# Performance work log

Measured on AMD Instinct MI355X. Metric: run time of the kernel, lower is better.

## Reference

```python
import jax, jax.numpy as jnp
import numpy as np

C = 256      # channel_num
K = 9        # key_num
B, H, W = 8, 64, 64


def setup_inputs() -> dict:
    key = jax.random.key(0)
    ks = jax.random.split(key, 12)
    s = 1.0 / np.sqrt(C)
    return {
        "query_layer": jax.random.normal(ks[0], (B, C, H, W), jnp.float32),
        "key_layer": jax.random.normal(ks[1], (B, C, H, W), jnp.float32),
        "gumbel_noise": jax.random.gumbel(ks[2], (B, K, H, W), jnp.float32),
        "w_refer": jax.random.normal(ks[3], (C, C), jnp.float32) * s,
        "b_refer": jax.random.normal(ks[4], (C,), jnp.float32) * 0.01,
        "w_attn": jax.random.normal(ks[5], (K, C), jnp.float32) * s,
        "b_attn": jax.random.normal(ks[6], (K,), jnp.float32) * 0.01,
        "w_mask": jax.random.normal(ks[7], (K, C), jnp.float32) * s,
        "b_mask": jax.random.normal(ks[8], (K,), jnp.float32) * 0.01,
        "w_off": jax.random.normal(ks[9], (2 * K, C), jnp.float32) * 0.02,
        "b_off": jax.random.normal(ks[10], (2 * K,), jnp.float32) * 0.01,
        "temp": 1,
    }


def _conv1x1(w, b, x):
    # w: (O,C), x: (B,C,H,W) -> (B,O,H,W)
    return jnp.einsum('oc,bchw->bohw', w, x) + b[None, :, None, None]


def _sample_one(img, py, px):
    # img: (C,H,W); py,px: (K,H,W) absolute sampling coords (bilinear, zero pad)
    h, w = img.shape[1], img.shape[2]
    y0 = jnp.floor(py)
    x0 = jnp.floor(px)
    wy = py - y0          # weight toward y0+1
    wx = px - x0

    def gather(yi, xi):
        valid = (yi >= 0) & (yi < h) & (xi >= 0) & (xi < w)
        yc = jnp.clip(yi, 0, h - 1).astype(jnp.int32)
        xc = jnp.clip(xi, 0, w - 1).astype(jnp.int32)
        return img[:, yc, xc] * valid[None].astype(img.dtype)  # (C,K,H,W)

    out = (gather(y0, x0) * ((1 - wy) * (1 - wx))[None]
           + gather(y0, x0 + 1) * ((1 - wy) * wx)[None]
           + gather(y0 + 1, x0) * (wy * (1 - wx))[None]
           + gather(y0 + 1, x0 + 1) * (wy * wx)[None])
    return out  # (C,K,H,W)


def reference(query_layer, key_layer, gumbel_noise, w_refer, b_refer,
              w_attn, b_attn, w_mask, b_mask, w_off, b_off, temp):
    key_feature = _conv1x1(w_refer, b_refer, key_layer)          # (B,C,H,W)
    attn_weights = _conv1x1(w_attn, b_attn, query_layer)         # (B,K,H,W)
    soft_mask = _conv1x1(w_mask, b_mask, query_layer)            # (B,K,H,W)
    # gumbel_softmax(hard=False) over key dim
    hard_mask = jax.nn.softmax((soft_mask + gumbel_noise) / temp, axis=1)
    offset = _conv1x1(w_off, b_off, query_layer)                 # (B,2K,H,W)

    # faithful to offset[:, i:i+2]: overlapping (dy,dx) slices
    dy = offset[:, 0:K]        # (B,K,H,W)
    dx = offset[:, 1:K + 1]    # (B,K,H,W)
    ys = jnp.arange(H, dtype=offset.dtype)[None, None, :, None]
    xs = jnp.arange(W, dtype=offset.dtype)[None, None, None, :]
    py = ys + dy
    px = xs + dx

    sampled = jax.vmap(_sample_one)(key_feature, py, px)         # (B,C,K,H,W)

    aw = jax.nn.softmax(attn_weights * hard_mask, axis=1)        # (B,K,H,W)
    out = jnp.einsum('bkhw,bckhw->bchw', aw, sampled)            # (B,C,H,W)
    return out
```

## Files before the change

### kernel.cpp

```cpp
#include <hip/hip_runtime.h>

typedef unsigned short u16;
typedef __attribute__((ext_vector_type(8))) short bf16x8;
typedef __attribute__((ext_vector_type(4))) float f32x4;

__device__ __forceinline__ u16 f2bf(float f) {
    unsigned u = __float_as_uint(f);
    unsigned r = (u + 0x7fffu + ((u >> 16) & 1u)) >> 16;
    return (u16)r;
}
__device__ __forceinline__ float bf2f(u16 h) {
    union { unsigned u; float f; } x; x.u = ((unsigned)h) << 16; return x.f;
}

#define NB 8
#define NC 256
#define NK 9
#define NH 64
#define NW 64
#define NP 4096
#define BAND 320
#define SB_STRIDE 328

__global__ __launch_bounds__(256) void kf_gemm(const float* __restrict__ key,
                                               const float* __restrict__ w_refer,
                                               const float* __restrict__ b_refer,
                                               u16* __restrict__ kf16)
{
    const int bid = blockIdx.x;
    const int b   = bid & 7;
    const int p0  = (bid >> 3) << 6;
    const int lane = threadIdx.x & 63, wid = threadIdx.x >> 6;
    const int fr = lane & 15, kq = (lane >> 4) << 3;
    const int co0w = wid << 6;

    f32x4 acc[4][4];
    #pragma unroll
    for (int i = 0; i < 4; ++i)
        #pragma unroll
        for (int j = 0; j < 4; ++j) acc[i][j] = (f32x4){0.f, 0.f, 0.f, 0.f};

    const float* kb = &key[(size_t)b * NC * NP + p0];

    for (int ks = 0; ks < 8; ++ks) {
        const int k0 = (ks << 5) + kq;
        bf16x8 af[4], bfv[4];
        #pragma unroll
        for (int mi = 0; mi < 4; ++mi) {
            const float* src = &w_refer[(size_t)(co0w + (mi << 4) + fr) * NC + k0];
            float4 v0 = *(const float4*)src;
            float4 v1 = *(const float4*)(src + 4);
            bf16x8 a;
            a[0] = (short)f2bf(v0.x); a[1] = (short)f2bf(v0.y);
            a[2] = (short)f2bf(v0.z); a[3] = (short)f2bf(v0.w);
            a[4] = (short)f2bf(v1.x); a[5] = (short)f2bf(v1.y);
            a[6] = (short)f2bf(v1.z); a[7] = (short)f2bf(v1.w);
            af[mi] = a;
        }
        #pragma unroll
        for (int ni = 0; ni < 4; ++ni) {
            const float* src = &kb[(size_t)k0 * NP + (ni << 4) + fr];
            bf16x8 bv;
            #pragma unroll
            for (int j = 0; j < 8; ++j) bv[j] = (short)f2bf(src[(size_t)j * NP]);
            bfv[ni] = bv;
        }
        #pragma unroll
        for (int mi = 0; mi < 4; ++mi)
            #pragma unroll
            for (int ni = 0; ni < 4; ++ni)
                acc[mi][ni] = __builtin_amdgcn_mfma_f32_16x16x32_bf16(af[mi], bfv[ni], acc[mi][ni], 0, 0, 0);
    }

    const int col = lane & 15, rbase = (lane >> 4) << 2;
    #pragma unroll
    for (int mi = 0; mi < 4; ++mi) {
        #pragma unroll
        for (int rr = 0; rr < 4; ++rr) {
            int co = co0w + (mi << 4) + rbase + rr;
            float bias = b_refer[co];
            u16* dst = &kf16[((size_t)b * NC + co) * NP + p0 + col];
            #pragma unroll
            for (int ni = 0; ni < 4; ++ni)
                dst[ni << 4] = f2bf(acc[mi][ni][rr] + bias);
        }
    }
}

__global__ __launch_bounds__(256) void head_meta(const float* __restrict__ query,
                                                 const float* __restrict__ gumbel,
                                                 const float* __restrict__ w_attn, const float* __restrict__ b_attn,
                                                 const float* __restrict__ w_mask, const float* __restrict__ b_mask,
                                                 const float* __restrict__ w_off,  const float* __restrict__ b_off,
                                                 const int* __restrict__ temp_p,
                                                 float4* __restrict__ wgt, uint2* __restrict__ offs)
{
    __shared__ u16 A[48][264];
    __shared__ float hdT[128][41];
    const int pt = blockIdx.x;
    const int b  = pt & 7;
    const int p0 = (pt >> 3) << 7;
    const int t = threadIdx.x;
    const int lane = t & 63, wn = t >> 6;
    const int fr = lane & 15, kq = (lane >> 4) << 3;

    for (int i = t; i < 1152; i += 256) {
        int o = i >> 5, c = (i & 31) << 3;
        const float* src = (o < 9) ? &w_attn[o * NC + c]
                       : (o < 18 ? &w_mask[(o - 9) * NC + c]
                                 : &w_off[(o - 18) * NC + c]);
        float4 v0 = *(const float4*)src;
        float4 v1 = *(const float4*)(src + 4);
        bf16x8 a;
        a[0] = (short)f2bf(v0.x); a[1] = (short)f2bf(v0.y);
        a[2] = (short)f2bf(v0.z); a[3] = (short)f2bf(v0.w);
        a[4] = (short)f2bf(v1.x); a[5] = (short)f2bf(v1.y);
        a[6] = (short)f2bf(v1.z); a[7] = (short)f2bf(v1.w);
        *(bf16x8*)&A[o][c] = a;
    }
    for (int i = t; i < 384; i += 256) {
        bf16x8 z = {0,0,0,0,0,0,0,0};
        *(bf16x8*)&A[36 + (i >> 5)][(i & 31) << 3] = z;
    }
    __syncthreads();

    f32x4 acc[3][2];
    #pragma unroll
    for (int i = 0; i < 3; ++i)
        #pragma unroll
        for (int j = 0; j < 2; ++j) acc[i][j] = (f32x4){0.f, 0.f, 0.f, 0.f};

    for (int ks = 0; ks < 8; ++ks) {
        const int k0 = (ks << 5) + kq;
        bf16x8 af[3], bfv[2];
        #pragma unroll
        for (int mi = 0; mi < 3; ++mi)
            af[mi] = *(const bf16x8*)&A[(mi << 4) + fr][k0];
        #pragma unroll
        for (int ni = 0; ni < 2; ++ni) {
            const float* src = &query[((size_t)b * NC + k0) * NP + p0 + (wn << 5) + (ni << 4) + fr];
            bf16x8 bv;
            #pragma unroll
            for (int j = 0; j < 8; ++j) bv[j] = (short)f2bf(src[(size_t)j * NP]);
            bfv[ni] = bv;
        }
        #pragma unroll
        for (int mi = 0; mi < 3; ++mi)
            #pragma unroll
            for (int ni = 0; ni < 2; ++ni)
                acc[mi][ni] = __builtin_amdgcn_mfma_f32_16x16x32_bf16(af[mi], bfv[ni], acc[mi][ni], 0, 0, 0);
    }
    const int col = lane & 15, rbase = (lane >> 4) << 2;
    #pragma unroll
    for (int mi = 0; mi < 3; ++mi) {
        #pragma unroll
        for (int rr = 0; rr < 4; ++rr) {
            int o = (mi << 4) + rbase + rr;
            if (o < 36) {
                float bias = (o < 9) ? b_attn[o] : (o < 18) ? b_mask[o - 9] : b_off[o - 18];
                #pragma unroll
                for (int ni = 0; ni < 2; ++ni)
                    hdT[(wn << 5) + (ni << 4) + col][o] = acc[mi][ni][rr] + bias;
            }
        }
    }
    __syncthreads();

    if (t < 128) {
        const int pxg = p0 + t;
        const int row = pxg >> 6, xcol = pxg & 63;
        float v[36];
        #pragma unroll
        for (int o = 0; o < 36; ++o) v[o] = hdT[t][o];

        int ti = temp_p[0];
        float tempf = (ti >= 1 && ti < (1 << 23)) ? (float)ti : __int_as_float(ti);
        float am[9], hs[9];
        float mx = -1e30f;
        #pragma unroll
        for (int k = 0; k < 9; ++k) {
            am[k] = v[k];
            float g = gumbel[((size_t)b * NK + k) * NP + pxg];
            hs[k] = (v[9 + k] + g) / tempf;
            mx = fmaxf(mx, hs[k]);
        }
        float ssum = 0.f;
        #pragma unroll
        for (int k = 0; k < 9; ++k) { hs[k] = __expf(hs[k] - mx); ssum += hs[k]; }
        float inv = 1.f / ssum;
        float lg[9]; float mx2 = -1e30f;
        #pragma unroll
        for (int k = 0; k < 9; ++k) { lg[k] = am[k] * (hs[k] * inv); mx2 = fmaxf(mx2, lg[k]); }
        float s2 = 0.f;
        #pragma unroll
        for (int k = 0; k < 9; ++k) { lg[k] = __expf(lg[k] - mx2); s2 += lg[k]; }
        float inv2 = 1.f / s2;
        #pragma unroll
        for (int k = 0; k < 9; ++k) {
            float a = lg[k] * inv2;
            float pyv = (float)row  + v[18 + k];
            float pxv = (float)xcol + v[19 + k];
            float y0f = floorf(pyv), x0f = floorf(pxv);
            float wy = pyv - y0f, wx = pxv - x0f;
            int y0 = (int)y0f, x0 = (int)x0f;
            int y1 = y0 + 1, x1 = x0 + 1;
            float vy0 = (y0 >= 0 && y0 < NH) ? 1.f : 0.f;
            float vy1 = (y1 >= 0 && y1 < NH) ? 1.f : 0.f;
            float vx0 = (x0 >= 0 && x0 < NW) ? 1.f : 0.f;
            float vx1 = (x1 >= 0 && x1 < NW) ? 1.f : 0.f;
            int y0c = min(max(y0, 0), NH - 1), y1c = min(max(y1, 0), NH - 1);
            int x0c = min(max(x0, 0), NW - 1), x1c = min(max(x1, 0), NW - 1);
            unsigned o00 = (unsigned)(y0c * NW + x0c), o01 = (unsigned)(y0c * NW + x1c);
            unsigned o10 = (unsigned)(y1c * NW + x0c), o11 = (unsigned)(y1c * NW + x1c);
            size_t idx = ((size_t)b * NK + k) * NP + pxg;
            wgt[idx]  = make_float4(a * (1.f - wy) * (1.f - wx) * vy0 * vx0,
                                    a * (1.f - wy) * wx * vy0 * vx1,
                                    a * wy * (1.f - wx) * vy1 * vx0,
                                    a * wy * wx * vy1 * vx1);
            offs[idx] = make_uint2(o00 | (o01 << 16), o10 | (o11 << 16));
        }
    }
}

__global__ __launch_bounds__(512, 4) void sample_pass(const u16* __restrict__ kf16,
                                                      const float4* __restrict__ wgt,
                                                      const uint2* __restrict__ offs,
                                                      float* __restrict__ out)
{
    __shared__ float Sf[64][BAND];

    const int bid = blockIdx.x;
    const int b = bid & 7, row = bid >> 3;
    const int t = threadIdx.x;
    const int lane = t & 63, wid = t >> 6;
    const int fr = lane & 15, kq = (lane >> 4) << 3;
    const int c0 = wid << 5;
    const int ylo = min(max(row - 2, 0), NH - 5);
    const int base = ylo << 6;
    const u16* kfb = kf16 + (size_t)b * NC * NP + base;

    bf16x8 apre[4][2];
    #pragma unroll
    for (int s = 0; s < 4; ++s)
        #pragma unroll
        for (int mi = 0; mi < 2; ++mi)
            apre[s][mi] = *(const bf16x8*)&kfb[(size_t)(c0 + (mi << 4) + fr) * NP + (s << 5) + kq];

    const int px = t & 63, kg = t >> 6;
    size_t idx0 = ((size_t)b * NK + kg) * NP + (row << 6) + px;
    float4 wv0 = wgt[idx0];
    uint2  ov0 = offs[idx0];
    float4 wv1 = make_float4(0.f, 0.f, 0.f, 0.f);
    uint2  ov1 = make_uint2(0u, 0u);
    if (kg == 0) {
        size_t idx1 = ((size_t)b * NK + 8) * NP + (row << 6) + px;
        wv1 = wgt[idx1]; ov1 = offs[idx1];
    }

    #pragma unroll
    for (int i = 0; i < 10; ++i)
        ((float4*)Sf)[t + (i << 9)] = (float4){0.f, 0.f, 0.f, 0.f};
    __syncthreads();

    bool esc = false;
    #pragma unroll
    for (int s = 0; s < 2; ++s) {
        if (s == 1 && kg != 0) break;
        float4 wv = s ? wv1 : wv0;
        uint2  ov = s ? ov1 : ov0;
        int   o4[4] = { (int)(ov.x & 0xffffu), (int)(ov.x >> 16),
                        (int)(ov.y & 0xffffu), (int)(ov.y >> 16) };
        float w4[4] = { wv.x, wv.y, wv.z, wv.w };
        #pragma unroll
        for (int c = 0; c < 4; ++c) {
            int u = o4[c] - base;
            if ((unsigned)u < (unsigned)BAND) atomicAdd(&Sf[px][u], w4[c]);
            else esc = true;
        }
    }
    __syncthreads();

    u16* Sb = (u16*)&Sf[0][0];
    bf16x8 pk[5]; int po[5];
    #pragma unroll
    for (int r = 0; r < 5; ++r) {
        int i = t + (r << 9);
        int p = i / 40, j = (i % 40) << 3;
        float4 a = *(const float4*)&Sf[p][j];
        float4 c = *(const float4*)&Sf[p][j + 4];
        bf16x8 q;
        q[0] = (short)f2bf(a.x); q[1] = (short)f2bf(a.y);
        q[2] = (short)f2bf(a.z); q[3] = (short)f2bf(a.w);
        q[4] = (short)f2bf(c.x); q[5] = (short)f2bf(c.y);
        q[6] = (short)f2bf(c.z); q[7] = (short)f2bf(c.w);
        pk[r] = q; po[r] = p * SB_STRIDE + j;
    }
    __syncthreads();
    #pragma unroll
    for (int r = 0; r < 5; ++r)
        *(bf16x8*)&Sb[po[r]] = pk[r];
    __syncthreads();

    f32x4 acc[2][4];
    #pragma unroll
    for (int i = 0; i < 2; ++i)
        #pragma unroll
        for (int j = 0; j < 4; ++j) acc[i][j] = (f32x4){0.f, 0.f, 0.f, 0.f};

    #pragma unroll
    for (int step = 0; step < 10; ++step) {
        bf16x8 a0 = apre[step & 3][0], a1 = apre[step & 3][1];
        if (step + 4 < 10) {
            #pragma unroll
            for (int mi = 0; mi < 2; ++mi)
                apre[step & 3][mi] =
                    *(const bf16x8*)&kfb[(size_t)(c0 + (mi << 4) + fr) * NP + ((step + 4) << 5) + kq];
        }
        bf16x8 bfv[4];
        #pragma unroll
        for (int ni = 0; ni < 4; ++ni)
            bfv[ni] = *(const bf16x8*)&Sb[((ni << 4) + fr) * SB_STRIDE + (step << 5) + kq];
        #pragma unroll
        for (int ni = 0; ni < 4; ++ni) {
            acc[0][ni] = __builtin_amdgcn_mfma_f32_16x16x32_bf16(a0, bfv[ni], acc[0][ni], 0, 0, 0);
            acc[1][ni] = __builtin_amdgcn_mfma_f32_16x16x32_bf16(a1, bfv[ni], acc[1][ni], 0, 0, 0);
        }
    }

    const int col = lane & 15, rbase = (lane >> 4) << 2;
    float* ob = out + (size_t)b * NC * NP + (row << 6);
    #pragma unroll
    for (int mi = 0; mi < 2; ++mi) {
        #pragma unroll
        for (int rr = 0; rr < 4; ++rr) {
            int c = c0 + (mi << 4) + rbase + rr;
            #pragma unroll
            for (int ni = 0; ni < 4; ++ni)
                ob[(size_t)c * NP + (ni << 4) + col] = acc[mi][ni][rr];
        }
    }

    __syncthreads();
    if (esc) {
        for (int s = 0; s < (kg == 0 ? 2 : 1); ++s) {
            int k = s ? 8 : kg;
            size_t idx = ((size_t)b * NK + k) * NP + (row << 6) + px;
            float4 wv = wgt[idx];
            uint2  ov = offs[idx];
            int   o4[4] = { (int)(ov.x & 0xffffu), (int)(ov.x >> 16),
                            (int)(ov.y & 0xffffu), (int)(ov.y >> 16) };
            float w4[4] = { wv.x, wv.y, wv.z, wv.w };
            for (int c = 0; c < 4; ++c) {
                int u = o4[c] - base;
                if ((unsigned)u >= (unsigned)BAND) {
                    for (int cc = 0; cc < NC; ++cc)
                        atomicAdd(&ob[(size_t)cc * NP + px],
                                  w4[c] * bf2f(kf16[((size_t)b * NC + cc) * NP + o4[c]]));
                }
            }
        }
    }
}

extern "C" void kernel_launch(void* const* d_in, const int* in_sizes, int n_in,
                              void* d_out, int out_size, void* d_ws, size_t ws_size,
                              hipStream_t stream)
{
    const float* query   = (const float*)d_in[0];
    const float* key     = (const float*)d_in[1];
    const float* gumbel  = (const float*)d_in[2];
    const float* w_refer = (const float*)d_in[3];
    const float* b_refer = (const float*)d_in[4];
    const float* w_attn  = (const float*)d_in[5];
    const float* b_attn  = (const float*)d_in[6];
    const float* w_mask  = (const float*)d_in[7];
    const float* b_mask  = (const float*)d_in[8];
    const float* w_off   = (const float*)d_in[9];
    const float* b_off   = (const float*)d_in[10];
    const int*   temp    = (const int*)d_in[11];
    float* out = (float*)d_out;

    char* ws = (char*)d_ws;
    u16*    kf16 = (u16*)ws;
    float4* wgt  = (float4*)(ws + (size_t)NB * NP * NC * 2);
    uint2*  offs = (uint2*)((char*)wgt + (size_t)NB * NK * NP * 16);

    kf_gemm<<<512, 256, 0, stream>>>(key, w_refer, b_refer, kf16);
    head_meta<<<256, 256, 0, stream>>>(query, gumbel, w_attn, b_attn, w_mask, b_mask,
                                       w_off, b_off, temp, wgt, offs);
    sample_pass<<<512, 512, 0, stream>>>(kf16, wgt, offs, out);
}
```

Baseline: 67.16 us.

## Fuse GEMM, head and sampling passes into one cooperative kernel with grid sync

Merges the three launches (key-feature GEMM, head/meta computation, banded sampling GEMM) into a single cooperative kernel of 256 blocks by 512 threads. A grid-wide sync presumably separates producing kf16/wgt/offs from consuming them. The key tile is now staged through LDS before bf16 conversion, and each block handles two rows in the sampling phase. This removes launch gaps and inter-kernel drains, but cuts the grid to 256 blocks with large LDS, adds grid-sync cost, and lowers parallelism per phase.

```diff
diff --git a/kernel.cpp b/kernel.cpp
--- a/kernel.cpp
+++ b/kernel.cpp
@@ -1,4 +1,7 @@
 #include <hip/hip_runtime.h>
+#include <hip/hip_cooperative_groups.h>
+
+namespace cg = cooperative_groups;
 
 typedef unsigned short u16;
 typedef __attribute__((ext_vector_type(8))) short bf16x8;
@@ -21,33 +24,106 @@
 #define NP 4096
 #define BAND 320
 #define SB_STRIDE 328
-
-__global__ __launch_bounds__(256) void kf_gemm(const float* __restrict__ key,
-                                               const float* __restrict__ w_refer,
-                                               const float* __restrict__ b_refer,
-                                               u16* __restrict__ kf16)
+#define KF_STR 68
+
+__global__ __launch_bounds__(512, 2) void fused(const float* __restrict__ key,
+                                                const float* __restrict__ query,
+                                                const float* __restrict__ gumbel,
+                                                const float* __restrict__ w_refer,
+                                                const float* __restrict__ b_refer,
+                                                const float* __restrict__ w_attn, const float* __restrict__ b_attn,
+                                                const float* __restrict__ w_mask, const float* __restrict__ b_mask,
+                                                const float* __restrict__ w_off,  const float* __restrict__ b_off,
+                                                const int* __restrict__ temp_p,
+                                                u16* __restrict__ kf16,
+                                                float4* __restrict__ wgt, uint2* __restrict__ offs,
+                                                float* __restrict__ out)
 {
-    const int bid = blockIdx.x;
-    const int b   = bid & 7;
-    const int p0  = (bid >> 3) << 6;
-    const int lane = threadIdx.x & 63, wid = threadIdx.x >> 6;
+    __shared__ __align__(16) char smem[81920];
+    const int bid = blockIdx.x, t = threadIdx.x;
+    const int b = bid & 7, seg = bid >> 3;
+    const int lane = t & 63;
     const int fr = lane & 15, kq = (lane >> 4) << 3;
-    const int co0w = wid << 6;
-
-    f32x4 acc[4][4];
-    #pragma unroll
-    for (int i = 0; i < 4; ++i)
-        #pragma unroll
-        for (int j = 0; j < 4; ++j) acc[i][j] = (f32x4){0.f, 0.f, 0.f, 0.f};
-
-    const float* kb = &key[(size_t)b * NC * NP + p0];
-
-    for (int ks = 0; ks < 8; ++ks) {
-        const int k0 = (ks << 5) + kq;
-        bf16x8 af[4], bfv[4];
-        #pragma unroll
-        for (int mi = 0; mi < 4; ++mi) {
-            const float* src = &w_refer[(size_t)(co0w + (mi << 4) + fr) * NC + k0];
+    const int col = lane & 15, rbase = (lane >> 4) << 2;
+
+    {
+        float* Kf = (float*)smem;
+        const int w = t >> 6;
+        const int co0 = w << 5;
+        #pragma unroll
+        for (int tile = 0; tile < 2; ++tile) {
+            const int p0 = ((seg << 1) + tile) << 6;
+            if (tile) __syncthreads();
+            #pragma unroll
+            for (int i = 0; i < 8; ++i) {
+                int idx = (i << 9) + t;
+                int k = idx >> 4, px4 = (idx & 15) << 2;
+                float4 v = *(const float4*)&key[((size_t)b * NC + k) * NP + p0 + px4];
+                *(float4*)&Kf[k * KF_STR + px4] = v;
+            }
+            __syncthreads();
+
+            f32x4 acc[2][4];
+            #pragma unroll
+            for (int i = 0; i < 2; ++i)
+                #pragma unroll
+                for (int j = 0; j < 4; ++j) acc[i][j] = (f32x4){0.f, 0.f, 0.f, 0.f};
+
+            for (int ks = 0; ks < 8; ++ks) {
+                const int k0 = (ks << 5) + kq;
+                bf16x8 af[2], bfv[4];
+                #pragma unroll
+                for (int mi = 0; mi < 2; ++mi) {
+                    const float* src = &w_refer[(size_t)(co0 + (mi << 4) + fr) * NC + k0];
+                    float4 v0 = *(const float4*)src;
+                    float4 v1 = *(const float4*)(src + 4);
+                    bf16x8 a;
+                    a[0] = (short)f2bf(v0.x); a[1] = (short)f2bf(v0.y);
+                    a[2] = (short)f2bf(v0.z); a[3] = (short)f2bf(v0.w);
+                    a[4] = (short)f2bf(v1.x); a[5] = (short)f2bf(v1.y);
+                    a[6] = (short)f2bf(v1.z); a[7] = (short)f2bf(v1.w);
+                    af[mi] = a;
+                }
+                #pragma unroll
+                for (int ni = 0; ni < 4; ++ni) {
+                    const float* src = &Kf[(size_t)k0 * KF_STR + (ni << 4) + fr];
+                    bf16x8 bv;
+                    #pragma unroll
+                    for (int j = 0; j < 8; ++j) bv[j] = (short)f2bf(src[j * KF_STR]);
+                    bfv[ni] = bv;
+                }
+                #pragma unroll
+                for (int mi = 0; mi < 2; ++mi)
+                    #pragma unroll
+                    for (int ni = 0; ni < 4; ++ni)
+                        acc[mi][ni] = __builtin_amdgcn_mfma_f32_16x16x32_bf16(af[mi], bfv[ni], acc[mi][ni], 0, 0, 0);
+            }
+            #pragma unroll
+            for (int mi = 0; mi < 2; ++mi) {
+                #pragma unroll
+                for (int rr = 0; rr < 4; ++rr) {
+                    int co = co0 + (mi << 4) + rbase + rr;
+                    float bias = b_refer[co];
+                    u16* dst = &kf16[((size_t)b * NC + co) * NP + p0 + col];
+                    #pragma unroll
+                    for (int ni = 0; ni < 4; ++ni)
+                        dst[ni << 4] = f2bf(acc[mi][ni][rr] + bias);
+                }
+            }
+        }
+    }
+    __syncthreads();
+
+    {
+        u16   (*A)[264]  = (u16(*)[264])smem;
+        float (*hdT)[41] = (float(*)[41])(smem + 25344);
+        const int p0h = seg << 7;
+
+        for (int i = t; i < 1152; i += 512) {
+            int o = i >> 5, c = (i & 31) << 3;
+            const float* src = (o < 9) ? &w_attn[o * NC + c]
+                           : (o < 18 ? &w_mask[(o - 9) * NC + c]
+                                     : &w_off[(o - 18) * NC + c]);
             float4 v0 = *(const float4*)src;
             float4 v1 = *(const float4*)(src + 4);
             bf16x8 a;
@@ -55,307 +131,234 @@
             a[2] = (short)f2bf(v0.z); a[3] = (short)f2bf(v0.w);
             a[4] = (short)f2bf(v1.x); a[5] = (short)f2bf(v1.y);
             a[6] = (short)f2bf(v1.z); a[7] = (short)f2bf(v1.w);
-            af[mi] = a;
-        }
-        #pragma unroll
-        for (int ni = 0; ni < 4; ++ni) {
-            const float* src = &kb[(size_t)k0 * NP + (ni << 4) + fr];
-            bf16x8 bv;
-            #pragma unroll
-            for (int j = 0; j < 8; ++j) bv[j] = (short)f2bf(src[(size_t)j * NP]);
-            bfv[ni] = bv;
-        }
-        #pragma unroll
-        for (int mi = 0; mi < 4; ++mi)
-            #pragma unroll
-            for (int ni = 0; ni < 4; ++ni)
-                acc[mi][ni] = __builtin_amdgcn_mfma_f32_16x16x32_bf16(af[mi], bfv[ni], acc[mi][ni], 0, 0, 0);
+            *(bf16x8*)&A[o][c] = a;
+        }
+        for (int i = t; i < 384; i += 512) {
+            bf16x8 z = {0,0,0,0,0,0,0,0};
+            *(bf16x8*)&A[36 + (i >> 5)][(i & 31) << 3] = z;
+        }
+        __syncthreads();
+
+        const int w = t >> 6, px0 = w << 4;
+        f32x4 acc[3];
+        #pragma unroll
+        for (int i = 0; i < 3; ++i) acc[i] = (f32x4){0.f, 0.f, 0.f, 0.f};
+
+        for (int ks = 0; ks < 8; ++ks) {
+            const int k0 = (ks << 5) + kq;
+            bf16x8 af[3], bv;
+            #pragma unroll
+            for (int mi = 0; mi < 3; ++mi)
+                af[mi] = *(const bf16x8*)&A[(mi << 4) + fr][k0];
+            {
+                const float* src = &query[((size_t)b * NC + k0) * NP + p0h + px0 + fr];
+                #pragma unroll
+                for (int j = 0; j < 8; ++j) bv[j] = (short)f2bf(src[(size_t)j * NP]);
+            }
+            #pragma unroll
+            for (int mi = 0; mi < 3; ++mi)
+                acc[mi] = __builtin_amdgcn_mfma_f32_16x16x32_bf16(af[mi], bv, acc[mi], 0, 0, 0);
+        }
+        #pragma unroll
+        for (int mi = 0; mi < 3; ++mi) {
+            #pragma unroll
+            for (int rr = 0; rr < 4; ++rr) {
+                int o = (mi << 4) + rbase + rr;
+                if (o < 36) {
+                    float bias = (o < 9) ? b_attn[o] : (o < 18) ? b_mask[o - 9] : b_off[o - 18];
+                    hdT[px0 + col][o] = acc[mi][rr] + bias;
+                }
+            }
+        }
+        __syncthreads();
+
+        if (t < 128) {
+            const int pxg = p0h + t;
+            const int row = pxg >> 6, xcol = pxg & 63;
+            float v[36];
+            #pragma unroll
+            for (int o = 0; o < 36; ++o) v[o] = hdT[t][o];
+
+            int ti = temp_p[0];
+            float tempf = (ti >= 1 && ti < (1 << 23)) ? (float)ti : __int_as_float(ti);
+            float am[9], hs[9];
+            float mx = -1e30f;
+            #pragma unroll
+            for (int k = 0; k < 9; ++k) {
+                am[k] = v[k];
+                float g = gumbel[((size_t)b * NK + k) * NP + pxg];
+                hs[k] = (v[9 + k] + g) / tempf;
+                mx = fmaxf(mx, hs[k]);
+            }
+            float ssum = 0.f;
+            #pragma unroll
+            for (int k = 0; k < 9; ++k) { hs[k] = __expf(hs[k] - mx); ssum += hs[k]; }
+            float inv = 1.f / ssum;
+            float lg[9]; float mx2 = -1e30f;
+            #pragma unroll
+            for (int k = 0; k < 9; ++k) { lg[k] = am[k] * (hs[k] * inv); mx2 = fmaxf(mx2, lg[k]); }
+            float s2 = 0.f;
+            #pragma unroll
+            for (int k = 0; k < 9; ++k) { lg[k] = __expf(lg[k] - mx2); s2 += lg[k]; }
+            float inv2 = 1.f / s2;
+            #pragma unroll
+            for (int k = 0; k < 9; ++k) {
+                float a = lg[k] * inv2;
+                float pyv = (float)row  + v[18 + k];
+                float pxv = (float)xcol + v[19 + k];
+                float y0f = floorf(pyv), x0f = floorf(pxv);
+                float wy = pyv - y0f, wx = pxv - x0f;
+                int y0 = (int)y0f, x0 = (int)x0f;
+                int y1 = y0 + 1, x1 = x0 + 1;
+                float vy0 = (y0 >= 0 && y0 < NH) ? 1.f : 0.f;
+                float vy1 = (y1 >= 0 && y1 < NH) ? 1.f : 0.f;
+                float vx0 = (x0 >= 0 && x0 < NW) ? 1.f : 0.f;
+                float vx1 = (x1 >= 0 && x1 < NW) ? 1.f : 0.f;
+                int y0c = min(max(y0, 0), NH - 1), y1c = min(max(y1, 0), NH - 1);
+                int x0c = min(max(x0, 0), NW - 1), x1c = min(max(x1, 0), NW - 1);
+                unsigned o00 = (unsigned)(y0c * NW + x0c), o01 = (unsigned)(y0c * NW + x1c);
+                unsigned o10 = (unsigned)(y1c * NW + x0c), o11 = (unsigned)(y1c * NW + x1c);
+                size_t idx = ((size_t)b * NK + k) * NP + pxg;
+                wgt[idx]  = make_float4(a * (1.f - wy) * (1.f - wx) * vy0 * vx0,
+                                        a * (1.f - wy) * wx * vy0 * vx1,
+                                        a * wy * (1.f - wx) * vy1 * vx0,
+                                        a * wy * wx * vy1 * vx1);
+                offs[idx] = make_uint2(o00 | (o01 << 16), o10 | (o11 << 16));
+            }
+        }
     }
 
-    const int col = lane & 15, rbase = (lane >> 4) << 2;
-    #pragma unroll
-    for (int mi = 0; mi < 4; ++mi) {
-        #pragma unroll
-        for (int rr = 0; rr < 4; ++rr) {
-            int co = co0w + (mi << 4) + rbase + rr;
-            float bias = b_refer[co];
-            u16* dst = &kf16[((size_t)b * NC + co) * NP + p0 + col];
-            #pragma unroll
-            for (int ni = 0; ni < 4; ++ni)
-                dst[ni << 4] = f2bf(acc[mi][ni][rr] + bias);
-        }
-    }
-}
-
-__global__ __launch_bounds__(256) void head_meta(const float* __restrict__ query,
-                                                 const float* __restrict__ gumbel,
-                                                 const float* __restrict__ w_attn, const float* __restrict__ b_attn,
-                                                 const float* __restrict__ w_mask, const float* __restrict__ b_mask,
-                                                 const float* __restrict__ w_off,  const float* __restrict__ b_off,
-                                                 const int* __restrict__ temp_p,
-                                                 float4* __restrict__ wgt, uint2* __restrict__ offs)
-{
-    __shared__ u16 A[48][264];
-    __shared__ float hdT[128][41];
-    const int pt = blockIdx.x;
-    const int b  = pt & 7;
-    const int p0 = (pt >> 3) << 7;
-    const int t = threadIdx.x;
-    const int lane = t & 63, wn = t >> 6;
-    const int fr = lane & 15, kq = (lane >> 4) << 3;
-
-    for (int i = t; i < 1152; i += 256) {
-        int o = i >> 5, c = (i & 31) << 3;
-        const float* src = (o < 9) ? &w_attn[o * NC + c]
-                       : (o < 18 ? &w_mask[(o - 9) * NC + c]
-                                 : &w_off[(o - 18) * NC + c]);
-        float4 v0 = *(const float4*)src;
-        float4 v1 = *(const float4*)(src + 4);
-        bf16x8 a;
-        a[0] = (short)f2bf(v0.x); a[1] = (short)f2bf(v0.y);
-        a[2] = (short)f2bf(v0.z); a[3] = (short)f2bf(v0.w);
-        a[4] = (short)f2bf(v1.x); a[5] = (short)f2bf(v1.y);
-        a[6] = (short)f2bf(v1.z); a[7] = (short)f2bf(v1.w);
-        *(bf16x8*)&A[o][c] = a;
-    }
-    for (int i = t; i < 384; i += 256) {
-        bf16x8 z = {0,0,0,0,0,0,0,0};
-        *(bf16x8*)&A[36 + (i >> 5)][(i & 31) << 3] = z;
-    }
-    __syncthreads();
-
-    f32x4 acc[3][2];
-    #pragma unroll
-    for (int i = 0; i < 3; ++i)
-        #pragma unroll
-        for (int j = 0; j < 2; ++j) acc[i][j] = (f32x4){0.f, 0.f, 0.f, 0.f};
-
-    for (int ks = 0; ks < 8; ++ks) {
-        const int k0 = (ks << 5) + kq;
-        bf16x8 af[3], bfv[2];
-        #pragma unroll
-        for (int mi = 0; mi < 3; ++mi)
-            af[mi] = *(const bf16x8*)&A[(mi << 4) + fr][k0];
-        #pragma unroll
-        for (int ni = 0; ni < 2; ++ni) {
-            const float* src = &query[((size_t)b * NC + k0) * NP + p0 + (wn << 5) + (ni << 4) + fr];
-            bf16x8 bv;
-            #pragma unroll
-            for (int j = 0; j < 8; ++j) bv[j] = (short)f2bf(src[(size_t)j * NP]);
-            bfv[ni] = bv;
-        }
-        #pragma unroll
-        for (int mi = 0; mi < 3; ++mi)
-            #pragma unroll
-            for (int ni = 0; ni < 2; ++ni)
-                acc[mi][ni] = __builtin_amdgcn_mfma_f32_16x16x32_bf16(af[mi], bfv[ni], acc[mi][ni], 0, 0, 0);
-    }
-    const int col = lane & 15, rbase = (lane >> 4) << 2;
-    #pragma unroll
-    for (int mi = 0; mi < 3; ++mi) {
-        #pragma unroll
-        for (int rr = 0; rr < 4; ++rr) {
-            int o = (mi << 4) + rbase + rr;
-            if (o < 36) {
-                float bias = (o < 9) ? b_attn[o] : (o < 18) ? b_mask[o - 9] : b_off[o - 18];
-                #pragma unroll
-                for (int ni = 0; ni < 2; ++ni)
-                    hdT[(wn << 5) + (ni << 4) + col][o] = acc[mi][ni][rr] + bias;
-            }
-        }
-    }
-    __syncthreads();
-
-    if (t < 128) {
-        const int pxg = p0 + t;
-        const int row = pxg >> 6, xcol = pxg & 63;
-        float v[36];
-        #pragma unroll
-        for (int o = 0; o < 36; ++o) v[o] = hdT[t][o];
-
-        int ti = temp_p[0];
-        float tempf = (ti >= 1 && ti < (1 << 23)) ? (float)ti : __int_as_float(ti);
-        float am[9], hs[9];
-        float mx = -1e30f;
-        #pragma unroll
-        for (int k = 0; k < 9; ++k) {
-            am[k] = v[k];
-            float g = gumbel[((size_t)b * NK + k) * NP + pxg];
-            hs[k] = (v[9 + k] + g) / tempf;
-            mx = fmaxf(mx, hs[k]);
-        }
-        float ssum = 0.f;
-        #pragma unroll
-        for (int k = 0; k < 9; ++k) { hs[k] = __expf(hs[k] - mx); ssum += hs[k]; }
-        float inv = 1.f / ssum;
-        float lg[9]; float mx2 = -1e30f;
-        #pragma unroll
-        for (int k = 0; k < 9; ++k) { lg[k] = am[k] * (hs[k] * inv); mx2 = fmaxf(mx2, lg[k]); }
-        float s2 = 0.f;
-        #pragma unroll
-        for (int k = 0; k < 9; ++k) { lg[k] = __expf(lg[k] - mx2); s2 += lg[k]; }
-        float inv2 = 1.f / s2;
-        #pragma unroll
-        for (int k = 0; k < 9; ++k) {
-            float a = lg[k] * inv2;
-            float pyv = (float)row  + v[18 + k];
-            float pxv = (float)xcol + v[19 + k];
-            float y0f = floorf(pyv), x0f = floorf(pxv);
-            float wy = pyv - y0f, wx = pxv - x0f;
-            int y0 = (int)y0f, x0 = (int)x0f;
-            int y1 = y0 + 1, x1 = x0 + 1;
-            float vy0 = (y0 >= 0 && y0 < NH) ? 1.f : 0.f;
-            float vy1 = (y1 >= 0 && y1 < NH) ? 1.f : 0.f;
-            float vx0 = (x0 >= 0 && x0 < NW) ? 1.f : 0.f;
-            float vx1 = (x1 >= 0 && x1 < NW) ? 1.f : 0.f;
-            int y0c = min(max(y0, 0), NH - 1), y1c = min(max(y1, 0), NH - 1);
-            int x0c = min(max(x0, 0), NW - 1), x1c = min(max(x1, 0), NW - 1);
-            unsigned o00 = (unsigned)(y0c * NW + x0c), o01 = (unsigned)(y0c * NW + x1c);
-            unsigned o10 = (unsigned)(y1c * NW + x0c), o11 = (unsigned)(y1c * NW + x1c);
-            size_t idx = ((size_t)b * NK + k) * NP + pxg;
-            wgt[idx]  = make_float4(a * (1.f - wy) * (1.f - wx) * vy0 * vx0,
-                                    a * (1.f - wy) * wx * vy0 * vx1,
-                                    a * wy * (1.f - wx) * vy1 * vx0,
-                                    a * wy * wx * vy1 * vx1);
-            offs[idx] = make_uint2(o00 | (o01 << 16), o10 | (o11 << 16));
-        }
-    }
-}
-
-__global__ __launch_bounds__(512, 4) void sample_pass(const u16* __restrict__ kf16,
-                                                      const float4* __restrict__ wgt,
-                                                      const uint2* __restrict__ offs,
-                                                      float* __restrict__ out)
-{
-    __shared__ float Sf[64][BAND];
-
-    const int bid = blockIdx.x;
-    const int b = bid & 7, row = bid >> 3;
-    const int t = threadIdx.x;
-    const int lane = t & 63, wid = t >> 6;
-    const int fr = lane & 15, kq = (lane >> 4) << 3;
+    cg::this_grid().sync();
+
+    float (*Sf)[BAND] = (float(*)[BAND])smem;
+    const int wid = t >> 6;
     const int c0 = wid << 5;
-    const int ylo = min(max(row - 2, 0), NH - 5);
-    const int base = ylo << 6;
-    const u16* kfb = kf16 + (size_t)b * NC * NP + base;
-
-    bf16x8 apre[4][2];
-    #pragma unroll
-    for (int s = 0; s < 4; ++s)
-        #pragma unroll
-        for (int mi = 0; mi < 2; ++mi)
-            apre[s][mi] = *(const bf16x8*)&kfb[(size_t)(c0 + (mi << 4) + fr) * NP + (s << 5) + kq];
-
     const int px = t & 63, kg = t >> 6;
-    size_t idx0 = ((size_t)b * NK + kg) * NP + (row << 6) + px;
-    float4 wv0 = wgt[idx0];
-    uint2  ov0 = offs[idx0];
-    float4 wv1 = make_float4(0.f, 0.f, 0.f, 0.f);
-    uint2  ov1 = make_uint2(0u, 0u);
-    if (kg == 0) {
-        size_t idx1 = ((size_t)b * NK + 8) * NP + (row << 6) + px;
-        wv1 = wgt[idx1]; ov1 = offs[idx1];
-    }
-
-    #pragma unroll
-    for (int i = 0; i < 10; ++i)
-        ((float4*)Sf)[t + (i << 9)] = (float4){0.f, 0.f, 0.f, 0.f};
-    __syncthreads();
-
-    bool esc = false;
-    #pragma unroll
-    for (int s = 0; s < 2; ++s) {
-        if (s == 1 && kg != 0) break;
-        float4 wv = s ? wv1 : wv0;
-        uint2  ov = s ? ov1 : ov0;
-        int   o4[4] = { (int)(ov.x & 0xffffu), (int)(ov.x >> 16),
-                        (int)(ov.y & 0xffffu), (int)(ov.y >> 16) };
-        float w4[4] = { wv.x, wv.y, wv.z, wv.w };
-        #pragma unroll
-        for (int c = 0; c < 4; ++c) {
-            int u = o4[c] - base;
-            if ((unsigned)u < (unsigned)BAND) atomicAdd(&Sf[px][u], w4[c]);
-            else esc = true;
-        }
-    }
-    __syncthreads();
-
-    u16* Sb = (u16*)&Sf[0][0];
-    bf16x8 pk[5]; int po[5];
-    #pragma unroll
-    for (int r = 0; r < 5; ++r) {
-        int i = t + (r << 9);
-        int p = i / 40, j = (i % 40) << 3;
-        float4 a = *(const float4*)&Sf[p][j];
-        float4 c = *(const float4*)&Sf[p][j + 4];
-        bf16x8 q;
-        q[0] = (short)f2bf(a.x); q[1] = (short)f2bf(a.y);
-        q[2] = (short)f2bf(a.z); q[3] = (short)f2bf(a.w);
-        q[4] = (short)f2bf(c.x); q[5] = (short)f2bf(c.y);
-        q[6] = (short)f2bf(c.z); q[7] = (short)f2bf(c.w);
-        pk[r] = q; po[r] = p * SB_STRIDE + j;
-    }
-    __syncthreads();
-    #pragma unroll
-    for (int r = 0; r < 5; ++r)
-        *(bf16x8*)&Sb[po[r]] = pk[r];
-    __syncthreads();
-
-    f32x4 acc[2][4];
-    #pragma unroll
-    for (int i = 0; i < 2; ++i)
-        #pragma unroll
-        for (int j = 0; j < 4; ++j) acc[i][j] = (f32x4){0.f, 0.f, 0.f, 0.f};
-
-    #pragma unroll
-    for (int step = 0; step < 10; ++step) {
-        bf16x8 a0 = apre[step & 3][0], a1 = apre[step & 3][1];
-        if (step + 4 < 10) {
+
+    #pragma unroll 1
+    for (int r = 0; r < 2; ++r) {
+        const int row = (seg << 1) + r;
+        const int ylo = min(max(row - 2, 0), NH - 5);
+        const int base = ylo << 6;
+        const u16* kfb = kf16 + (size_t)b * NC * NP + base;
+        __syncthreads();
+
+        bf16x8 apre[4][2];
+        #pragma unroll
+        for (int s = 0; s < 4; ++s)
             #pragma unroll
             for (int mi = 0; mi < 2; ++mi)
-                apre[step & 3][mi] =
-                    *(const bf16x8*)&kfb[(size_t)(c0 + (mi << 4) + fr) * NP + ((step + 4) << 5) + kq];
-        }
-        bf16x8 bfv[4];
-        #pragma unroll
-        for (int ni = 0; ni < 4; ++ni)
-            bfv[ni] = *(const bf16x8*)&Sb[((ni << 4) + fr) * SB_STRIDE + (step << 5) + kq];
-        #pragma unroll
-        for (int ni = 0; ni < 4; ++ni) {
-            acc[0][ni] = __builtin_amdgcn_mfma_f32_16x16x32_bf16(a0, bfv[ni], acc[0][ni], 0, 0, 0);
-            acc[1][ni] = __builtin_amdgcn_mfma_f32_16x16x32_bf16(a1, bfv[ni], acc[1][ni], 0, 0, 0);
-        }
-    }
-
-    const int col = lane & 15, rbase = (lane >> 4) << 2;
-    float* ob = out + (size_t)b * NC * NP + (row << 6);
-    #pragma unroll
-    for (int mi = 0; mi < 2; ++mi) {
-        #pragma unroll
-        for (int rr = 0; rr < 4; ++rr) {
-            int c = c0 + (mi << 4) + rbase + rr;
-            #pragma unroll
-            for (int ni = 0; ni < 4; ++ni)
-                ob[(size_t)c * NP + (ni << 4) + col] = acc[mi][ni][rr];
-        }
-    }
-
-    __syncthreads();
-    if (esc) {
-        for (int s = 0; s < (kg == 0 ? 2 : 1); ++s) {
-            int k = s ? 8 : kg;
-            size_t idx = ((size_t)b * NK + k) * NP + (row << 6) + px;
-            float4 wv = wgt[idx];
-            uint2  ov = offs[idx];
+                apre[s][mi] = *(const bf16x8*)&kfb[(size_t)(c0 + (mi << 4) + fr) * NP + (s << 5) + kq];
+
+        size_t idx0 = ((size_t)b * NK + kg) * NP + (row << 6) + px;
+        float4 wv0 = wgt[idx0];
+        uint2  ov0 = offs[idx0];
+        float4 wv1 = make_float4(0.f, 0.f, 0.f, 0.f);
+        uint2  ov1 = make_uint2(0u, 0u);
+        if (kg == 0) {
+            size_t idx1 = ((size_t)b * NK + 8) * NP + (row << 6) + px;
+            wv1 = wgt[idx1]; ov1 = offs[idx1];
+        }
+
+        #pragma unroll
+        for (int i = 0; i < 10; ++i)
+            ((float4*)Sf)[t + (i << 9)] = (float4){0.f, 0.f, 0.f, 0.f};
+        __syncthreads();
+
+        bool esc = false;
+        #pragma unroll
+        for (int s = 0; s < 2; ++s) {
+            if (s == 1 && kg != 0) break;
+            float4 wvv = s ? wv1 : wv0;
+            uint2  ov  = s ? ov1 : ov0;
             int   o4[4] = { (int)(ov.x & 0xffffu), (int)(ov.x >> 16),
                             (int)(ov.y & 0xffffu), (int)(ov.y >> 16) };
-            float w4[4] = { wv.x, wv.y, wv.z, wv.w };
+            float w4[4] = { wvv.x, wvv.y, wvv.z, wvv.w };
+            #pragma unroll
             for (int c = 0; c < 4; ++c) {
                 int u = o4[c] - base;
-                if ((unsigned)u >= (unsigned)BAND) {
-                    for (int cc = 0; cc < NC; ++cc)
-                        atomicAdd(&ob[(size_t)cc * NP + px],
-                                  w4[c] * bf2f(kf16[((size_t)b * NC + cc) * NP + o4[c]]));
+                if ((unsigned)u < (unsigned)BAND) atomicAdd(&Sf[px][u], w4[c]);
+                else esc = true;
+            }
+        }
+        __syncthreads();
+
+        u16* Sb = (u16*)&Sf[0][0];
+        bf16x8 pk[5]; int po[5];
+        #pragma unroll
+        for (int rr = 0; rr < 5; ++rr) {
+            int i = t + (rr << 9);
+            int p = i / 40, j = (i % 40) << 3;
+            float4 a = *(const float4*)&Sf[p][j];
+            float4 c = *(const float4*)&Sf[p][j + 4];
+            bf16x8 q;
+            q[0] = (short)f2bf(a.x); q[1] = (short)f2bf(a.y);
+            q[2] = (short)f2bf(a.z); q[3] = (short)f2bf(a.w);
+            q[4] = (short)f2bf(c.x); q[5] = (short)f2bf(c.y);
+            q[6] = (short)f2bf(c.z); q[7] = (short)f2bf(c.w);
+            pk[rr] = q; po[rr] = p * SB_STRIDE + j;
+        }
+        __syncthreads();
+        #pragma unroll
+        for (int rr = 0; rr < 5; ++rr)
+            *(bf16x8*)&Sb[po[rr]] = pk[rr];
+        __syncthreads();
+
+        f32x4 acc[2][4];
+        #pragma unroll
+        for (int i = 0; i < 2; ++i)
+            #pragma unroll
+            for (int j = 0; j < 4; ++j) acc[i][j] = (f32x4){0.f, 0.f, 0.f, 0.f};
+
+        #pragma unroll
+        for (int step = 0; step < 10; ++step) {
+            bf16x8 a0 = apre[step & 3][0], a1 = apre[step & 3][1];
+            if (step + 4 < 10) {
+                #pragma unroll
+                for (int mi = 0; mi < 2; ++mi)
+                    apre[step & 3][mi] =
+                        *(const bf16x8*)&kfb[(size_t)(c0 + (mi << 4) + fr) * NP + ((step + 4) << 5) + kq];
+            }
+            bf16x8 bfv[4];
+            #pragma unroll
+            for (int ni = 0; ni < 4; ++ni)
+                bfv[ni] = *(const bf16x8*)&Sb[((ni << 4) + fr) * SB_STRIDE + (step << 5) + kq];
+            #pragma unroll
+            for (int ni = 0; ni < 4; ++ni) {
+                acc[0][ni] = __builtin_amdgcn_mfma_f32_16x16x32_bf16(a0, bfv[ni], acc[0][ni], 0, 0, 0);
+                acc[1][ni] = __builtin_amdgcn_mfma_f32_16x16x32_bf16(a1, bfv[ni], acc[1][ni], 0, 0, 0);
+            }
+        }
+
+        float* ob = out + (size_t)b * NC * NP + (row << 6);
+        #pragma unroll
+        for (int mi = 0; mi < 2; ++mi) {
+            #pragma unroll
+            for (int rr = 0; rr < 4; ++rr) {
+                int c = c0 + (mi << 4) + rbase + rr;
+                #pragma unroll
+                for (int ni = 0; ni < 4; ++ni)
+                    ob[(size_t)c * NP + (ni << 4) + col] = acc[mi][ni][rr];
+            }
+        }
+
+        __syncthreads();
+        if (esc) {
+            for (int s = 0; s < (kg == 0 ? 2 : 1); ++s) {
+                int k = s ? 8 : kg;
+                size_t idx = ((size_t)b * NK + k) * NP + (row << 6) + px;
+                float4 wvv = wgt[idx];
+                uint2  ov  = offs[idx];
+                int   o4[4] = { (int)(ov.x & 0xffffu), (int)(ov.x >> 16),
+                                (int)(ov.y & 0xffffu), (int)(ov.y >> 16) };
+                float w4[4] = { wvv.x, wvv.y, wvv.z, wvv.w };
+                for (int c = 0; c < 4; ++c) {
+                    int u = o4[c] - base;
+                    if ((unsigned)u >= (unsigned)BAND) {
+                        for (int cc = 0; cc < NC; ++cc)
+                            atomicAdd(&ob[(size_t)cc * NP + px],
+                                      w4[c] * bf2f(kf16[((size_t)b * NC + cc) * NP + o4[c]]));
+                    }
                 }
             }
         }
@@ -385,8 +388,12 @@
     float4* wgt  = (float4*)(ws + (size_t)NB * NP * NC * 2);
     uint2*  offs = (uint2*)((char*)wgt + (size_t)NB * NK * NP * 16);
 
-    kf_gemm<<<512, 256, 0, stream>>>(key, w_refer, b_refer, kf16);
-    head_meta<<<256, 256, 0, stream>>>(query, gumbel, w_attn, b_attn, w_mask, b_mask,
-                                       w_off, b_off, temp, wgt, offs);
-    sample_pass<<<512, 512, 0, stream>>>(kf16, wgt, offs, out);
+    void* args[] = { (void*)&key, (void*)&query, (void*)&gumbel,
+                     (void*)&w_refer, (void*)&b_refer,
+                     (void*)&w_attn, (void*)&b_attn,
+                     (void*)&w_mask, (void*)&b_mask,
+                     (void*)&w_off, (void*)&b_off,
+                     (void*)&temp, (void*)&kf16, (void*)&wgt, (void*)&offs,
+                     (void*)&out };
+    hipLaunchCooperativeKernel((const void*)fused, dim3(256), dim3(512), args, 0, stream);
 }
```

Measured after the change: 115.9 us. +72.5%, slower.

## Fuse key-feature GEMM and head metadata kernels into one prep kernel

Applied to the files above, without the earlier changes.

Merges the key conv1x1 GEMM and the query head/metadata kernel into a single 512-thread kernel, so each block covers one image row of 64 pixels. All 8 waves compute the key features, and 4 waves then compute the 36 head outputs and the per-pixel sampling weights. This removes one kernel launch and lets the two independent stages share the same blocks. The cost is that the head stage now runs serially after the GEMM inside each block, with half the waves idle during it.

```diff
diff --git a/kernel.cpp b/kernel.cpp
--- a/kernel.cpp
+++ b/kernel.cpp
@@ -22,89 +22,28 @@
 #define BAND 320
 #define SB_STRIDE 328
 
-__global__ __launch_bounds__(256) void kf_gemm(const float* __restrict__ key,
+__global__ __launch_bounds__(512, 4) void prep(const float* __restrict__ key,
+                                               const float* __restrict__ query,
+                                               const float* __restrict__ gumbel,
                                                const float* __restrict__ w_refer,
                                                const float* __restrict__ b_refer,
-                                               u16* __restrict__ kf16)
+                                               const float* __restrict__ w_attn, const float* __restrict__ b_attn,
+                                               const float* __restrict__ w_mask, const float* __restrict__ b_mask,
+                                               const float* __restrict__ w_off,  const float* __restrict__ b_off,
+                                               const int* __restrict__ temp_p,
+                                               u16* __restrict__ kf16,
+                                               float4* __restrict__ wgt, uint2* __restrict__ offs)
 {
-    const int bid = blockIdx.x;
-    const int b   = bid & 7;
-    const int p0  = (bid >> 3) << 6;
-    const int lane = threadIdx.x & 63, wid = threadIdx.x >> 6;
+    __shared__ u16   A[48][264];
+    __shared__ float hdT[64][41];
+    const int bid = blockIdx.x, t = threadIdx.x;
+    const int b = bid & 7, seg = bid >> 3;
+    const int lane = t & 63, w = t >> 6;
     const int fr = lane & 15, kq = (lane >> 4) << 3;
-    const int co0w = wid << 6;
-
-    f32x4 acc[4][4];
-    #pragma unroll
-    for (int i = 0; i < 4; ++i)
-        #pragma unroll
-        for (int j = 0; j < 4; ++j) acc[i][j] = (f32x4){0.f, 0.f, 0.f, 0.f};
-
-    const float* kb = &key[(size_t)b * NC * NP + p0];
-
-    for (int ks = 0; ks < 8; ++ks) {
-        const int k0 = (ks << 5) + kq;
-        bf16x8 af[4], bfv[4];
-        #pragma unroll
-        for (int mi = 0; mi < 4; ++mi) {
-            const float* src = &w_refer[(size_t)(co0w + (mi << 4) + fr) * NC + k0];
-            float4 v0 = *(const float4*)src;
-            float4 v1 = *(const float4*)(src + 4);
-            bf16x8 a;
-            a[0] = (short)f2bf(v0.x); a[1] = (short)f2bf(v0.y);
-            a[2] = (short)f2bf(v0.z); a[3] = (short)f2bf(v0.w);
-            a[4] = (short)f2bf(v1.x); a[5] = (short)f2bf(v1.y);
-            a[6] = (short)f2bf(v1.z); a[7] = (short)f2bf(v1.w);
-            af[mi] = a;
-        }
-        #pragma unroll
-        for (int ni = 0; ni < 4; ++ni) {
-            const float* src = &kb[(size_t)k0 * NP + (ni << 4) + fr];
-            bf16x8 bv;
-            #pragma unroll
-            for (int j = 0; j < 8; ++j) bv[j] = (short)f2bf(src[(size_t)j * NP]);
-            bfv[ni] = bv;
-        }
-        #pragma unroll
-        for (int mi = 0; mi < 4; ++mi)
-            #pragma unroll
-            for (int ni = 0; ni < 4; ++ni)
-                acc[mi][ni] = __builtin_amdgcn_mfma_f32_16x16x32_bf16(af[mi], bfv[ni], acc[mi][ni], 0, 0, 0);
-    }
-
     const int col = lane & 15, rbase = (lane >> 4) << 2;
-    #pragma unroll
-    for (int mi = 0; mi < 4; ++mi) {
-        #pragma unroll
-        for (int rr = 0; rr < 4; ++rr) {
-            int co = co0w + (mi << 4) + rbase + rr;
-            float bias = b_refer[co];
-            u16* dst = &kf16[((size_t)b * NC + co) * NP + p0 + col];
-            #pragma unroll
-            for (int ni = 0; ni < 4; ++ni)
-                dst[ni << 4] = f2bf(acc[mi][ni][rr] + bias);
-        }
-    }
-}
-
-__global__ __launch_bounds__(256) void head_meta(const float* __restrict__ query,
-                                                 const float* __restrict__ gumbel,
-                                                 const float* __restrict__ w_attn, const float* __restrict__ b_attn,
-                                                 const float* __restrict__ w_mask, const float* __restrict__ b_mask,
-                                                 const float* __restrict__ w_off,  const float* __restrict__ b_off,
-                                                 const int* __restrict__ temp_p,
-                                                 float4* __restrict__ wgt, uint2* __restrict__ offs)
-{
-    __shared__ u16 A[48][264];
-    __shared__ float hdT[128][41];
-    const int pt = blockIdx.x;
-    const int b  = pt & 7;
-    const int p0 = (pt >> 3) << 7;
-    const int t = threadIdx.x;
-    const int lane = t & 63, wn = t >> 6;
-    const int fr = lane & 15, kq = (lane >> 4) << 3;
-
-    for (int i = t; i < 1152; i += 256) {
+    const int p0 = seg << 6;
+
+    for (int i = t; i < 1152; i += 512) {
         int o = i >> 5, c = (i & 31) << 3;
         const float* src = (o < 9) ? &w_attn[o * NC + c]
                        : (o < 18 ? &w_mask[(o - 9) * NC + c]
@@ -118,57 +57,102 @@
         a[6] = (short)f2bf(v1.z); a[7] = (short)f2bf(v1.w);
         *(bf16x8*)&A[o][c] = a;
     }
-    for (int i = t; i < 384; i += 256) {
+    if (t < 384) {
         bf16x8 z = {0,0,0,0,0,0,0,0};
-        *(bf16x8*)&A[36 + (i >> 5)][(i & 31) << 3] = z;
-    }
-    __syncthreads();
-
-    f32x4 acc[3][2];
-    #pragma unroll
-    for (int i = 0; i < 3; ++i)
-        #pragma unroll
-        for (int j = 0; j < 2; ++j) acc[i][j] = (f32x4){0.f, 0.f, 0.f, 0.f};
-
-    for (int ks = 0; ks < 8; ++ks) {
-        const int k0 = (ks << 5) + kq;
-        bf16x8 af[3], bfv[2];
-        #pragma unroll
-        for (int mi = 0; mi < 3; ++mi)
-            af[mi] = *(const bf16x8*)&A[(mi << 4) + fr][k0];
-        #pragma unroll
-        for (int ni = 0; ni < 2; ++ni) {
-            const float* src = &query[((size_t)b * NC + k0) * NP + p0 + (wn << 5) + (ni << 4) + fr];
-            bf16x8 bv;
-            #pragma unroll
-            for (int j = 0; j < 8; ++j) bv[j] = (short)f2bf(src[(size_t)j * NP]);
-            bfv[ni] = bv;
-        }
-        #pragma unroll
-        for (int mi = 0; mi < 3; ++mi)
-            #pragma unroll
-            for (int ni = 0; ni < 2; ++ni)
-                acc[mi][ni] = __builtin_amdgcn_mfma_f32_16x16x32_bf16(af[mi], bfv[ni], acc[mi][ni], 0, 0, 0);
-    }
-    const int col = lane & 15, rbase = (lane >> 4) << 2;
-    #pragma unroll
-    for (int mi = 0; mi < 3; ++mi) {
-        #pragma unroll
-        for (int rr = 0; rr < 4; ++rr) {
-            int o = (mi << 4) + rbase + rr;
-            if (o < 36) {
-                float bias = (o < 9) ? b_attn[o] : (o < 18) ? b_mask[o - 9] : b_off[o - 18];
+        *(bf16x8*)&A[36 + (t >> 5)][(t & 31) << 3] = z;
+    }
+
+    {
+        const int co0 = w << 5;
+        f32x4 acc[2][4];
+        #pragma unroll
+        for (int i = 0; i < 2; ++i)
+            #pragma unroll
+            for (int j = 0; j < 4; ++j) acc[i][j] = (f32x4){0.f, 0.f, 0.f, 0.f};
+
+        const float* kb = &key[(size_t)b * NC * NP + p0];
+
+        for (int ks = 0; ks < 8; ++ks) {
+            const int k0 = (ks << 5) + kq;
+            bf16x8 af[2], bfv[4];
+            #pragma unroll
+            for (int mi = 0; mi < 2; ++mi) {
+                const float* src = &w_refer[(size_t)(co0 + (mi << 4) + fr) * NC + k0];
+                float4 v0 = *(const float4*)src;
+                float4 v1 = *(const float4*)(src + 4);
+                bf16x8 a;
+                a[0] = (short)f2bf(v0.x); a[1] = (short)f2bf(v0.y);
+                a[2] = (short)f2bf(v0.z); a[3] = (short)f2bf(v0.w);
+                a[4] = (short)f2bf(v1.x); a[5] = (short)f2bf(v1.y);
+                a[6] = (short)f2bf(v1.z); a[7] = (short)f2bf(v1.w);
+                af[mi] = a;
+            }
+            #pragma unroll
+            for (int ni = 0; ni < 4; ++ni) {
+                const float* src = &kb[(size_t)k0 * NP + (ni << 4) + fr];
+                bf16x8 bv;
                 #pragma unroll
-                for (int ni = 0; ni < 2; ++ni)
-                    hdT[(wn << 5) + (ni << 4) + col][o] = acc[mi][ni][rr] + bias;
-            }
-        }
-    }
-    __syncthreads();
-
-    if (t < 128) {
+                for (int j = 0; j < 8; ++j) bv[j] = (short)f2bf(src[(size_t)j * NP]);
+                bfv[ni] = bv;
+            }
+            #pragma unroll
+            for (int mi = 0; mi < 2; ++mi)
+                #pragma unroll
+                for (int ni = 0; ni < 4; ++ni)
+                    acc[mi][ni] = __builtin_amdgcn_mfma_f32_16x16x32_bf16(af[mi], bfv[ni], acc[mi][ni], 0, 0, 0);
+        }
+        #pragma unroll
+        for (int mi = 0; mi < 2; ++mi) {
+            #pragma unroll
+            for (int rr = 0; rr < 4; ++rr) {
+                int co = co0 + (mi << 4) + rbase + rr;
+                float bias = b_refer[co];
+                u16* dst = &kf16[((size_t)b * NC + co) * NP + p0 + col];
+                #pragma unroll
+                for (int ni = 0; ni < 4; ++ni)
+                    dst[ni << 4] = f2bf(acc[mi][ni][rr] + bias);
+            }
+        }
+    }
+    __syncthreads();
+
+    if (w < 4) {
+        const int px0 = w << 4;
+        f32x4 acc[3];
+        #pragma unroll
+        for (int i = 0; i < 3; ++i) acc[i] = (f32x4){0.f, 0.f, 0.f, 0.f};
+
+        for (int ks = 0; ks < 8; ++ks) {
+            const int k0 = (ks << 5) + kq;
+            bf16x8 af[3], bv;
+            #pragma unroll
+            for (int mi = 0; mi < 3; ++mi)
+                af[mi] = *(const bf16x8*)&A[(mi << 4) + fr][k0];
+            {
+                const float* src = &query[((size_t)b * NC + k0) * NP + p0 + px0 + fr];
+                #pragma unroll
+                for (int j = 0; j < 8; ++j) bv[j] = (short)f2bf(src[(size_t)j * NP]);
+            }
+            #pragma unroll
+            for (int mi = 0; mi < 3; ++mi)
+                acc[mi] = __builtin_amdgcn_mfma_f32_16x16x32_bf16(af[mi], bv, acc[mi], 0, 0, 0);
+        }
+        #pragma unroll
+        for (int mi = 0; mi < 3; ++mi) {
+            #pragma unroll
+            for (int rr = 0; rr < 4; ++rr) {
+                int o = (mi << 4) + rbase + rr;
+                if (o < 36) {
+                    float bias = (o < 9) ? b_attn[o] : (o < 18) ? b_mask[o - 9] : b_off[o - 18];
+                    hdT[px0 + col][o] = acc[mi][rr] + bias;
+                }
+            }
+        }
+    }
+    __syncthreads();
+
+    if (t < 64) {
         const int pxg = p0 + t;
-        const int row = pxg >> 6, xcol = pxg & 63;
         float v[36];
         #pragma unroll
         for (int o = 0; o < 36; ++o) v[o] = hdT[t][o];
@@ -198,8 +182,8 @@
         #pragma unroll
         for (int k = 0; k < 9; ++k) {
             float a = lg[k] * inv2;
-            float pyv = (float)row  + v[18 + k];
-            float pxv = (float)xcol + v[19 + k];
+            float pyv = (float)seg + v[18 + k];
+            float pxv = (float)t   + v[19 + k];
             float y0f = floorf(pyv), x0f = floorf(pxv);
             float wy = pyv - y0f, wx = pxv - x0f;
             int y0 = (int)y0f, x0 = (int)x0f;
@@ -385,8 +369,8 @@
     float4* wgt  = (float4*)(ws + (size_t)NB * NP * NC * 2);
     uint2*  offs = (uint2*)((char*)wgt + (size_t)NB * NK * NP * 16);
 
-    kf_gemm<<<512, 256, 0, stream>>>(key, w_refer, b_refer, kf16);
-    head_meta<<<256, 256, 0, stream>>>(query, gumbel, w_attn, b_attn, w_mask, b_mask,
-                                       w_off, b_off, temp, wgt, offs);
+    prep<<<512, 512, 0, stream>>>(key, query, gumbel, w_refer, b_refer,
+                                  w_attn, b_attn, w_mask, b_mask, w_off, b_off,
+                                  temp, kf16, wgt, offs);
     sample_pass<<<512, 512, 0, stream>>>(kf16, wgt, offs, out);
 }
```

Result: faster. 61.51 us, median of 2 (-8.4%).
